# Kernel optimization log

Hardware: AMD Instinct MI355X
Metric: run time of the kernel (lower is better)

## Reference

```python
import jax, jax.numpy as jnp
import numpy as np

B, T, D = 2, 2048, 1024
H, d = 16, 64
INNER = H * d
K = 4  # conv_size
EPS_RMS = 1e-6
EPS_NORM = 1e-12


def _dconv(x, w, b):
    # depthwise causal conv: x (B,T,C), w (C,K), b (C,)
    xp = jnp.pad(x, ((0, 0), (K - 1, 0), (0, 0)))
    Tt = x.shape[1]
    out = b
    for k in range(K):
        out = out + xp[:, k:k + Tt] * w[:, k]
    return out


def _l2norm(x):
    n = jnp.sqrt(jnp.sum(x * x, axis=-1, keepdims=True))
    return x / jnp.maximum(n, EPS_NORM)


def setup_inputs() -> dict:
    key = jax.random.key(0)
    ks = jax.random.split(key, 12)
    s = 0.02
    inp = {
        'x': jax.random.normal(ks[0], (B, T, D), jnp.float32),
        'Wq': jax.random.normal(ks[1], (D, INNER), jnp.float32) * s,
        'Wk': jax.random.normal(ks[2], (D, INNER), jnp.float32) * s,
        'Wv': jax.random.normal(ks[3], (D, INNER), jnp.float32) * s,
        'Wa': jax.random.normal(ks[4], (D, H), jnp.float32) * s,
        'ba': jnp.full((H,), 2.0, jnp.float32),
        'Wb': jax.random.normal(ks[5], (D, H), jnp.float32) * s,
        'bb': jnp.zeros((H,), jnp.float32),
        'Wg': jax.random.normal(ks[6], (D, INNER), jnp.float32) * s,
        'Wo': jax.random.normal(ks[7], (INNER, D), jnp.float32) * s,
        'cq_w': jax.random.normal(ks[8], (INNER, K), jnp.float32) * 0.3,
        'cq_b': jnp.zeros((INNER,), jnp.float32),
        'ck_w': jax.random.normal(ks[9], (INNER, K), jnp.float32) * 0.3,
        'ck_b': jnp.zeros((INNER,), jnp.float32),
        'cv_w': jax.random.normal(ks[10], (INNER, K), jnp.float32) * 0.3,
        'cv_b': jnp.zeros((INNER,), jnp.float32),
        'gamma': jnp.zeros((INNER,), jnp.float32),
    }
    return inp


def reference(x, Wq, Wk, Wv, Wa, ba, Wb, bb, Wg, Wo,
              cq_w, cq_b, ck_w, ck_b, cv_w, cv_b, gamma):
    q = jax.nn.silu(_dconv(x @ Wq, cq_w, cq_b))
    k = jax.nn.silu(_dconv(x @ Wk, ck_w, ck_b))
    v = jax.nn.silu(_dconv(x @ Wv, cv_w, cv_b))
    q = _l2norm(q.reshape(B, T, H, d))
    k = _l2norm(k.reshape(B, T, H, d))
    v = v.reshape(B, T, H, d)
    alpha = jax.nn.sigmoid(x @ Wa + ba)  # (B,T,H)
    beta = jax.nn.sigmoid(x @ Wb + bb)   # (B,T,H)
    gate = jax.nn.silu(x @ Wg)           # (B,T,INNER)

    I_d = jnp.eye(d, dtype=x.dtype)

    def step(S, ins):
        q_t, k_t, v_t, a_t, b_t = ins  # q/k/v: (B,H,d); a,b: (B,H)
        a = a_t[..., None, None]
        b = b_t[..., None, None]
        kkT = k_t[..., :, None] * k_t[..., None, :]   # (B,H,d,d)
        vkT = v_t[..., :, None] * k_t[..., None, :]
        decay = a * (I_d - b * kkT)
        S = jnp.matmul(S, decay) + b * vkT
        o = jnp.einsum('bhde,bhe->bhd', S, q_t)
        return S, o

    # time-major scan inputs
    qT = jnp.transpose(q, (1, 0, 2, 3))
    kT = jnp.transpose(k, (1, 0, 2, 3))
    vT = jnp.transpose(v, (1, 0, 2, 3))
    aT = jnp.transpose(alpha, (1, 0, 2))
    bT = jnp.transpose(beta, (1, 0, 2))
    S0 = jnp.zeros((B, H, d, d), x.dtype)
    _, oT = jax.lax.scan(step, S0, (qT, kT, vT, aT, bT))  # (T,B,H,d)

    out = jnp.transpose(oT, (1, 0, 2, 3)).reshape(B, T, INNER)
    rms = jnp.sqrt(jnp.mean(out * out, axis=-1, keepdims=True) + EPS_RMS)
    out = out / rms * (1.0 + gamma)
    out = out * gate
    return out @ Wo
```

## Files before the change

### kernel.cpp

```cpp
#include <hip/hip_runtime.h>
#include <hip/hip_bf16.h>
#include <cmath>

#define B_ 2
#define T_ 2048
#define D_ 1024
#define H_ 16
#define DH 64
#define INNER_ 1024
#define BT (B_*T_)
#define NCH 32
#define NU (B_*H_*NCH)

typedef __attribute__((ext_vector_type(8))) __bf16 bf16x8;
typedef __attribute__((ext_vector_type(4))) float f32x4;
typedef const __attribute__((address_space(1))) unsigned gas_u32;
typedef __attribute__((address_space(3))) unsigned las_u32;

__device__ __forceinline__ void async16(const void* g, void* l) {
  __builtin_amdgcn_global_load_lds((gas_u32*)g, (las_u32*)l, 16, 0, 0);
}

__device__ __forceinline__ ushort bfr(float x) {
  __hip_bfloat16 t = __float2bfloat16(x);
  return *(ushort*)&t;
}
__device__ __forceinline__ void st_bf4(__hip_bfloat16* p, float a, float b, float c, float d) {
  ushort4 u; u.x = bfr(a); u.y = bfr(b); u.z = bfr(c); u.w = bfr(d);
  *(ushort4*)p = u;
}

__global__ __launch_bounds__(256) void cvt_bf16_kernel(const float* __restrict__ in,
                                                       __hip_bfloat16* __restrict__ out,
                                                       int n4) {
  int i = blockIdx.x * 256 + threadIdx.x;
  if (i >= n4) return;
  float4 v = *(const float4*)(in + (size_t)i * 4);
  __hip_bfloat16 t[4];
  t[0] = __float2bfloat16(v.x); t[1] = __float2bfloat16(v.y);
  t[2] = __float2bfloat16(v.z); t[3] = __float2bfloat16(v.w);
  *(uint2*)(out + (size_t)i * 4) = *(uint2*)t;
}

__global__ __launch_bounds__(256) void transpose_cvt_kernel(const float* __restrict__ in,
                                                            __hip_bfloat16* __restrict__ out,
                                                            int R, int C) {
  __shared__ float tile[32][33];
  const int bc = blockIdx.x * 32, br = blockIdx.y * 32;
  const int tx = threadIdx.x & 31, ty = threadIdx.x >> 5;
#pragma unroll
  for (int i = 0; i < 32; i += 8)
    tile[ty + i][tx] = in[(size_t)(br + ty + i) * C + bc + tx];
  __syncthreads();
#pragma unroll
  for (int i = 0; i < 32; i += 8)
    out[(size_t)(bc + ty + i) * R + br + tx] = __float2bfloat16(tile[tx][ty + i]);
}

__global__ __launch_bounds__(256) void wab_kernel(const float* __restrict__ Wa,
                                                  const float* __restrict__ Wb,
                                                  __hip_bfloat16* __restrict__ Wabt) {
  int idx = blockIdx.x * 256 + threadIdx.x;
  int j = idx >> 10, k = idx & 1023;
  float v = 0.f;
  if (j < 16) v = Wa[k * 16 + j];
  else if (j < 32) v = Wb[k * 16 + (j - 16)];
  Wabt[idx] = __float2bfloat16(v);
}

__global__ __launch_bounds__(256) void gemm_ab(const __hip_bfloat16* __restrict__ A,
                                               const __hip_bfloat16* __restrict__ Bt,
                                               const float* __restrict__ ba,
                                               const float* __restrict__ bb2,
                                               float* __restrict__ alpha,
                                               float* __restrict__ beta, int K) {
  __shared__ __hip_bfloat16 As[128 * 32];
  __shared__ __hip_bfloat16 Bs[128 * 32];
  const int tid = threadIdx.x;
  const int lane = tid & 63, wave = tid >> 6;
  const int wr = wave >> 1, wc = wave & 1;
  const int m0 = blockIdx.y * 128;
  const int srow = tid >> 2, skoff = (tid & 3) * 8;
  const int l15 = lane & 15, lg = lane >> 4;

  f32x4 acc[4][2];
#pragma unroll
  for (int m = 0; m < 4; ++m)
#pragma unroll
    for (int n = 0; n < 2; ++n) acc[m][n] = (f32x4)0.f;

  char* asB = (char*)As;
  char* bsB = (char*)Bs;
  const int ldsw = wave * 1024;

  for (int k0 = 0; k0 < K; k0 += 32) {
    async16(A + (size_t)(m0 + srow) * K + k0 + skoff, asB + ldsw);
    async16(A + (size_t)(m0 + 64 + srow) * K + k0 + skoff, asB + 4096 + ldsw);
    async16(Bt + (size_t)srow * K + k0 + skoff, bsB + ldsw);
    async16(Bt + (size_t)(64 + srow) * K + k0 + skoff, bsB + 4096 + ldsw);
    __syncthreads();
    if (wc == 0) {
      bf16x8 af[4], bfg[2];
#pragma unroll
      for (int m = 0; m < 4; ++m)
        af[m] = *(const bf16x8*)(asB + ((wr * 64 + m * 16 + l15) * 32 + lg * 8) * 2);
#pragma unroll
      for (int n = 0; n < 2; ++n)
        bfg[n] = *(const bf16x8*)(bsB + ((n * 16 + l15) * 32 + lg * 8) * 2);
#pragma unroll
      for (int m = 0; m < 4; ++m)
#pragma unroll
        for (int n = 0; n < 2; ++n)
          acc[m][n] = __builtin_amdgcn_mfma_f32_16x16x32_bf16(af[m], bfg[n], acc[m][n], 0, 0, 0);
    }
    __syncthreads();
  }
  if (wc != 0) return;
#pragma unroll
  for (int m = 0; m < 4; ++m) {
    const int rbase = m0 + wr * 64 + m * 16 + lg * 4;
#pragma unroll
    for (int n = 0; n < 2; ++n) {
      const float bias = (n == 0) ? ba[l15] : bb2[l15];
      float* dst = (n == 0) ? alpha : beta;
#pragma unroll
      for (int r = 0; r < 4; ++r) {
        float vv = acc[m][n][r] + bias;
        dst[(size_t)(rbase + r) * H_ + l15] = 1.f / (1.f + expf(-vv));
      }
    }
  }
}

__device__ __forceinline__ bf16x8 pfrag(const __hip_bfloat16* buf, int row, int ks, int lg) {
  return *(const bf16x8*)((const char*)buf + row * 128 + ks * 64 + lg * 16);
}

__global__ __launch_bounds__(512, 2) void gemm256(const __hip_bfloat16* __restrict__ A,
                                                  const __hip_bfloat16* __restrict__ Bt,
                                                  float* __restrict__ C,
                                                  int M, int N, int K, int act) {
  __shared__ __hip_bfloat16 As[2][256 * 64];
  __shared__ __hip_bfloat16 Bs[2][256 * 64];
  const int tid = threadIdx.x;
  const int lane = tid & 63, wv = tid >> 6;
  const int wr = wv >> 2, wc = wv & 3;
  const int m0 = blockIdx.y * 256, n0 = blockIdx.x * 256;
  const int l15 = lane & 15, lg = lane >> 4;
  const int sr8 = lane >> 3, sc = (lane & 7) * 8;

  f32x4 acc[8][4];
#pragma unroll
  for (int m = 0; m < 8; ++m)
#pragma unroll
    for (int n = 0; n < 4; ++n) acc[m][n] = (f32x4)0.f;

  auto stage = [&](int kt, int bsel) {
    const size_t k0 = (size_t)kt * 64;
    const __hip_bfloat16* Ab = A + (size_t)(m0 + wv * 8 + sr8) * K + k0 + sc;
    const __hip_bfloat16* Bb = Bt + (size_t)(n0 + wv * 8 + sr8) * K + k0 + sc;
    char* al = (char*)As[bsel] + wv * 1024;
    char* bl = (char*)Bs[bsel] + wv * 1024;
#pragma unroll
    for (int q = 0; q < 4; ++q) {
      async16(Ab + (size_t)q * 64 * K, al + q * 8192);
      async16(Bb + (size_t)q * 64 * K, bl + q * 8192);
    }
  };

  const int NT = K >> 6;
  stage(0, 0);
  __syncthreads();
  int cur = 0;
  for (int kt = 0; kt < NT; ++kt) {
    if (kt + 1 < NT) stage(kt + 1, cur ^ 1);
#pragma unroll
    for (int ks = 0; ks < 2; ++ks) {
      bf16x8 af[8], bfg[4];
#pragma unroll
      for (int m = 0; m < 8; ++m)
        af[m] = pfrag(As[cur], wr * 128 + m * 16 + l15, ks, lg);
#pragma unroll
      for (int n = 0; n < 4; ++n)
        bfg[n] = pfrag(Bs[cur], wc * 64 + n * 16 + l15, ks, lg);
#pragma unroll
      for (int m = 0; m < 8; ++m)
#pragma unroll
        for (int n = 0; n < 4; ++n)
          acc[m][n] = __builtin_amdgcn_mfma_f32_16x16x32_bf16(af[m], bfg[n], acc[m][n], 0, 0, 0);
    }
    __syncthreads();
    cur ^= 1;
  }

#pragma unroll
  for (int m = 0; m < 8; ++m) {
    const int rbase = m0 + wr * 128 + m * 16 + lg * 4;
#pragma unroll
    for (int n = 0; n < 4; ++n) {
      const int col = n0 + wc * 64 + n * 16 + l15;
      if (act == 2) {
        const int which = col >> 10;
        const int ncol = col & 1023;
        float* dst = C + (size_t)which * ((size_t)BT * INNER_) +
                     (size_t)rbase * 1024 + ncol;
#pragma unroll
        for (int r = 0; r < 4; ++r) {
          float vv = acc[m][n][r];
          if (which == 3) vv = vv / (1.f + expf(-vv));
          dst[(size_t)r * 1024] = vv;
        }
      } else {
#pragma unroll
        for (int r = 0; r < 4; ++r)
          C[(size_t)(rbase + r) * N + col] = acc[m][n][r];
      }
    }
  }
}

__global__ __launch_bounds__(256) void convnorm_kernel(
    const float* __restrict__ qpre, const float* __restrict__ kpre, const float* __restrict__ vpre,
    const float* __restrict__ cqw, const float* __restrict__ cqb,
    const float* __restrict__ ckw, const float* __restrict__ ckb,
    const float* __restrict__ cvw, const float* __restrict__ cvb,
    float* __restrict__ qn, float* __restrict__ kn, float* __restrict__ vn) {
  const int bt = blockIdx.x;
  const int t = bt & (T_ - 1);
  const int tid = threadIdx.x;
  const int c = tid * 4;

  auto run = [&](const float* __restrict__ pre, const float* __restrict__ w,
                 const float* __restrict__ bias, float* __restrict__ out, bool norm) {
    float r[4];
    float4 bv = *(const float4*)(bias + c);
    r[0] = bv.x; r[1] = bv.y; r[2] = bv.z; r[3] = bv.w;
    float wl[4][4];
#pragma unroll
    for (int i = 0; i < 4; ++i) {
      float4 wv = *(const float4*)(w + (size_t)(c + i) * 4);
      wl[i][0] = wv.x; wl[i][1] = wv.y; wl[i][2] = wv.z; wl[i][3] = wv.w;
    }
#pragma unroll
    for (int kk = 0; kk < 4; ++kk) {
      int tt = t - 3 + kk;
      if (tt >= 0) {
        float4 xv = *(const float4*)(pre + (size_t)(bt - 3 + kk) * INNER_ + c);
        float xa[4] = {xv.x, xv.y, xv.z, xv.w};
#pragma unroll
        for (int i = 0; i < 4; ++i) r[i] += xa[i] * wl[i][kk];
      }
    }
#pragma unroll
    for (int i = 0; i < 4; ++i) r[i] = r[i] / (1.f + expf(-r[i]));
    if (norm) {
      float ss = r[0]*r[0] + r[1]*r[1] + r[2]*r[2] + r[3]*r[3];
      ss += __shfl_xor(ss, 1); ss += __shfl_xor(ss, 2);
      ss += __shfl_xor(ss, 4); ss += __shfl_xor(ss, 8);
      float n = sqrtf(ss);
      float sc = 1.f / fmaxf(n, 1e-12f);
#pragma unroll
      for (int i = 0; i < 4; ++i) r[i] *= sc;
    }
    float4 ov = {r[0], r[1], r[2], r[3]};
    *(float4*)(out + (size_t)bt * INNER_ + c) = ov;
  };

  run(qpre, cqw, cqb, qn, true);
  run(kpre, ckw, ckb, kn, true);
  run(vpre, cvw, cvb, vn, false);
}

#define BST 72

__device__ __forceinline__ bf16x8 fragld(const __hip_bfloat16* buf, int row, int kk, int lg) {
  return *(const bf16x8*)(buf + row * BST + kk * 32 + lg * 8);
}

__global__ __launch_bounds__(256, 2) void precomp_kernel(
    const float* __restrict__ qn, const float* __restrict__ kn, const float* __restrict__ vn,
    const float* __restrict__ alpha, const float* __restrict__ beta,
    __hip_bfloat16* __restrict__ Zg, __hip_bfloat16* __restrict__ G2g,
    float* __restrict__ AVg, float* __restrict__ G1g, float* __restrict__ P63g) {
  __shared__ __hip_bfloat16 sKb[64 * BST], sKip[64 * BST], sKipT[64 * BST];
  __shared__ __hip_bfloat16 sQp[64 * BST], sAttn[64 * BST];
  __shared__ __hip_bfloat16 sXT[128 * BST];
  __shared__ __hip_bfloat16 sM[64 * BST];
  __shared__ float sMd[4][16][16];
  __shared__ float sP[64], sIP[64], sBP[64], sB[64];

  const int u = blockIdx.x;
  const int bh = u >> 5, c = u & 31;
  const int b = bh >> 4, h = bh & 15;
  const int tid = threadIdx.x, lane = tid & 63, wv = tid >> 6;
  const int l15 = lane & 15, lg = lane >> 4;
  const size_t bt0 = (size_t)b * T_ + (size_t)c * 64;
  const size_t hofs = (size_t)h * DH;

  if (wv == 0) {
    float a = alpha[(bt0 + lane) * H_ + h];
    float bb = beta[(bt0 + lane) * H_ + h];
    float la = logf(a);
#pragma unroll
    for (int d = 1; d < 64; d <<= 1) {
      float y = __shfl_up(la, d);
      if (lane >= d) la += y;
    }
    float P = expf(la);
    sP[lane] = P;
    sIP[lane] = 1.f / P;
    sBP[lane] = bb * P;
    sB[lane] = bb;
    if (lane == 63) P63g[u] = P;
  }
  __syncthreads();

#pragma unroll
  for (int i = 0; i < 4; ++i) {
    int e = tid + i * 256;
    int row = e >> 4, c4 = (e & 15) * 4;
    size_t g = (bt0 + row) * INNER_ + hofs + c4;
    float4 kv = *(const float4*)(kn + g);
    float4 qv = *(const float4*)(qn + g);
    float4 vv = *(const float4*)(vn + g);
    float bp = sBP[row], ip = sIP[row], pp = sP[row], bo = sB[row];
    st_bf4(&sKb[row * BST + c4], kv.x * bp, kv.y * bp, kv.z * bp, kv.w * bp);
    st_bf4(&sKip[row * BST + c4], kv.x * ip, kv.y * ip, kv.z * ip, kv.w * ip);
    st_bf4(&sQp[row * BST + c4], qv.x * pp, qv.y * pp, qv.z * pp, qv.w * pp);
    sKipT[(c4 + 0) * BST + row] = __float2bfloat16(kv.x * ip);
    sKipT[(c4 + 1) * BST + row] = __float2bfloat16(kv.y * ip);
    sKipT[(c4 + 2) * BST + row] = __float2bfloat16(kv.z * ip);
    sKipT[(c4 + 3) * BST + row] = __float2bfloat16(kv.w * ip);
    sXT[(c4 + 0) * BST + row] = __float2bfloat16(kv.x * bp);
    sXT[(c4 + 1) * BST + row] = __float2bfloat16(kv.y * bp);
    sXT[(c4 + 2) * BST + row] = __float2bfloat16(kv.z * bp);
    sXT[(c4 + 3) * BST + row] = __float2bfloat16(kv.w * bp);
    sXT[(64 + c4 + 0) * BST + row] = __float2bfloat16(vv.x * bo);
    sXT[(64 + c4 + 1) * BST + row] = __float2bfloat16(vv.y * bo);
    sXT[(64 + c4 + 2) * BST + row] = __float2bfloat16(vv.z * bo);
    sXT[(64 + c4 + 3) * BST + row] = __float2bfloat16(vv.w * bo);
  }
  __syncthreads();

  if (wv < 2) {
#pragma unroll
    for (int tt = wv * 2; tt < wv * 2 + 2; ++tt) {
      for (int n = 0; n <= tt; ++n) {
        f32x4 acc = (f32x4)0.f;
#pragma unroll
        for (int kk = 0; kk < 2; ++kk)
          acc = __builtin_amdgcn_mfma_f32_16x16x32_bf16(
              fragld(sKb, tt * 16 + l15, kk, lg), fragld(sKip, n * 16 + l15, kk, lg), acc, 0, 0, 0);
        if (n < tt) {
#pragma unroll
          for (int q = 0; q < 4; ++q)
            sM[(tt * 16 + lg * 4 + q) * BST + n * 16 + l15] = __float2bfloat16(acc[q]);
        } else {
#pragma unroll
          for (int q = 0; q < 4; ++q) {
            int rr = lg * 4 + q;
            sMd[tt][rr][l15] = (l15 < rr) ? acc[q] : 0.f;
            sM[(tt * 16 + rr) * BST + tt * 16 + l15] = __float2bfloat16(0.f);
          }
        }
      }
    }
  } else {
#pragma unroll
    for (int tt = (wv - 2) * 2; tt < (wv - 2) * 2 + 2; ++tt) {
      for (int n = 0; n < 4; ++n) {
        if (n <= tt) {
          f32x4 acc = (f32x4)0.f;
#pragma unroll
          for (int kk = 0; kk < 2; ++kk)
            acc = __builtin_amdgcn_mfma_f32_16x16x32_bf16(
                fragld(sQp, tt * 16 + l15, kk, lg), fragld(sKip, n * 16 + l15, kk, lg), acc, 0, 0, 0);
#pragma unroll
          for (int q = 0; q < 4; ++q) {
            int r = tt * 16 + lg * 4 + q, cl = n * 16 + l15;
            sAttn[r * BST + cl] = __float2bfloat16((cl <= r) ? acc[q] : 0.f);
          }
        } else {
#pragma unroll
          for (int q = 0; q < 4; ++q)
            sAttn[(tt * 16 + lg * 4 + q) * BST + n * 16 + l15] = __float2bfloat16(0.f);
        }
      }
    }
  }
  __syncthreads();

  auto diag_solve = [&](int I) {
    if (wv < 2) {
      const int cc = wv * 64 + lane;
      float x[16];
#pragma unroll
      for (int t = 0; t < 16; ++t) {
        float r = __bfloat162float(sXT[cc * BST + I * 16 + t]);
#pragma unroll
        for (int s = 0; s < t; ++s) r -= sMd[I][t][s] * x[s];
        x[t] = r;
        sXT[cc * BST + I * 16 + t] = __float2bfloat16(r);
      }
    }
  };

  diag_solve(0);
  __syncthreads();
#pragma unroll
  for (int I = 1; I < 4; ++I) {
    const int KK = (I == 3) ? 2 : 1;
#pragma unroll
    for (int ct2 = 0; ct2 < 2; ++ct2) {
      const int ct = wv * 2 + ct2;
      f32x4 uacc = (f32x4)0.f;
#pragma unroll
      for (int kk = 0; kk < KK; ++kk)
        uacc = __builtin_amdgcn_mfma_f32_16x16x32_bf16(
            fragld(sXT, ct * 16 + l15, kk, lg), fragld(sM, I * 16 + l15, kk, lg), uacc, 0, 0, 0);
#pragma unroll
      for (int q = 0; q < 4; ++q) {
        const int cc = ct * 16 + lg * 4 + q, t = I * 16 + l15;
        float old = __bfloat162float(sXT[cc * BST + t]);
        sXT[cc * BST + t] = __float2bfloat16(old - uacc[q]);
      }
    }
    __syncthreads();
    diag_solve(I);
    __syncthreads();
  }

  const float p63 = sP[63];
  const int tt = wv;
  const size_t go = (size_t)u * 4096;
#pragma unroll
  for (int n = 0; n < 4; ++n) {
    f32x4 av = (f32x4)0.f, aw = (f32x4)0.f, g1 = (f32x4)0.f, g2 = (f32x4)0.f;
#pragma unroll
    for (int kk = 0; kk < 2; ++kk) {
      bf16x8 at = fragld(sAttn, tt * 16 + l15, kk, lg);
      bf16x8 kt = fragld(sKipT, tt * 16 + l15, kk, lg);
      bf16x8 bv = fragld(sXT, 64 + n * 16 + l15, kk, lg);
      bf16x8 bw = fragld(sXT, n * 16 + l15, kk, lg);
      av = __builtin_amdgcn_mfma_f32_16x16x32_bf16(at, bv, av, 0, 0, 0);
      aw = __builtin_amdgcn_mfma_f32_16x16x32_bf16(at, bw, aw, 0, 0, 0);
      g1 = __builtin_amdgcn_mfma_f32_16x16x32_bf16(kt, bv, g1, 0, 0, 0);
      g2 = __builtin_amdgcn_mfma_f32_16x16x32_bf16(kt, bw, g2, 0, 0, 0);
    }
#pragma unroll
    for (int q = 0; q < 4; ++q) {
      int r = tt * 16 + lg * 4 + q, cl = n * 16 + l15;
      AVg[go + r * 64 + cl] = av[q];
      float qp = __bfloat162float(sQp[r * BST + cl]);
      Zg[go + r * 64 + cl] = __float2bfloat16(qp - aw[q]);
      G1g[go + cl * 64 + r] = p63 * g1[q];
      G2g[go + r * 64 + cl] = __float2bfloat16(p63 * g2[q]);
    }
  }
}

__device__ __forceinline__ bf16x8 sfrag(const __hip_bfloat16* buf, int row, int kk, int lg) {
  int byte = row * 128 + kk * 64 + lg * 16;
  byte ^= (row & 7) << 4;
  return *(const bf16x8*)((const char*)buf + byte);
}

__global__ __launch_bounds__(256) void chunkrec_kernel(
    const __hip_bfloat16* __restrict__ Zg, const __hip_bfloat16* __restrict__ G2g,
    const float* __restrict__ AVg, const float* __restrict__ G1g,
    const float* __restrict__ P63g, float* __restrict__ o) {
  __shared__ __align__(16) __hip_bfloat16 sR[16 * 64];
  __shared__ __align__(16) __hip_bfloat16 sZ[2][64 * 64];
  __shared__ __align__(16) __hip_bfloat16 sG2[2][64 * 64];
  const int blk = blockIdx.x;
  const int bh = blk >> 2;
  const int jb = blk & 3;
  const int b = bh >> 4, h = bh & 15;
  const int tid = threadIdx.x, lane = tid & 63, wv = tid >> 6;
  const int l15 = lane & 15, lg = lane >> 4;
  const size_t btb = (size_t)b * T_;
  const size_t hofs = (size_t)h * DH;

  f32x4 R = (f32x4)0.f;

  uint4 zr[2], gr[2];
  const int e0 = tid * 2;

  auto issue = [&](int c) {
    size_t ub = ((size_t)bh * NCH + c) * 4096;
#pragma unroll
    for (int i = 0; i < 2; ++i) {
      zr[i] = *(const uint4*)(Zg + ub + (size_t)(e0 + i) * 8);
      gr[i] = *(const uint4*)(G2g + ub + (size_t)(e0 + i) * 8);
    }
  };
  auto commit = [&](int buf) {
#pragma unroll
    for (int i = 0; i < 2; ++i) {
      int e = e0 + i;
      int row = e >> 3, colb = (e & 7) * 16;
      int byte = (row * 128 + colb) ^ ((row & 7) << 4);
      *(uint4*)((char*)sZ[buf] + byte) = zr[i];
      *(uint4*)((char*)sG2[buf] + byte) = gr[i];
    }
  };

  issue(0);
  commit(0);
  int cur = 0;
  for (int c = 0; c < NCH; ++c) {
#pragma unroll
    for (int q = 0; q < 4; ++q) {
      int i = lg * 4 + q;
      int byte = (i * 128 + (wv * 16 + l15) * 2) ^ ((i & 7) << 4);
      *(__hip_bfloat16*)((char*)sR + byte) = __float2bfloat16(R[q]);
    }
    __syncthreads();

    const size_t ub = ((size_t)bh * NCH + c) * 4096;
    float avr[4], g1r[4];
#pragma unroll
    for (int q = 0; q < 4; ++q) {
      int t = wv * 16 + lg * 4 + q;
      avr[q] = AVg[ub + t * 64 + jb * 16 + l15];
      g1r[q] = G1g[ub + (jb * 16 + lg * 4 + q) * 64 + wv * 16 + l15];
    }
    float p63 = P63g[(size_t)bh * NCH + c];
    if (c + 1 < NCH) issue(c + 1);

    bf16x8 zA[2], rF[2], gB[2];
#pragma unroll
    for (int kk = 0; kk < 2; ++kk) {
      zA[kk] = sfrag(sZ[cur], wv * 16 + l15, kk, lg);
      rF[kk] = sfrag(sR, l15, kk, lg);
      gB[kk] = sfrag(sG2[cur], wv * 16 + l15, kk, lg);
    }
    f32x4 oacc = (f32x4)0.f, gacc = (f32x4)0.f;
#pragma unroll
    for (int kk = 0; kk < 2; ++kk) {
      oacc = __builtin_amdgcn_mfma_f32_16x16x32_bf16(zA[kk], rF[kk], oacc, 0, 0, 0);
      gacc = __builtin_amdgcn_mfma_f32_16x16x32_bf16(rF[kk], gB[kk], gacc, 0, 0, 0);
    }
#pragma unroll
    for (int q = 0; q < 4; ++q) {
      int t = wv * 16 + lg * 4 + q;
      o[(btb + (size_t)c * 64 + t) * INNER_ + hofs + jb * 16 + l15] = avr[q] + oacc[q];
      R[q] = p63 * R[q] + g1r[q] - gacc[q];
    }
    __syncthreads();
    if (c + 1 < NCH) commit(cur ^ 1);
    cur ^= 1;
  }
}

__global__ __launch_bounds__(256) void rmsgate_kernel(const float* __restrict__ o,
    const float* __restrict__ gate, const float* __restrict__ gamma,
    __hip_bfloat16* __restrict__ outn) {
  const int bt = blockIdx.x;
  const int tid = threadIdx.x;
  const size_t base = (size_t)bt * INNER_ + tid * 4;
  float4 ov = *(const float4*)(o + base);
  float ss = ov.x*ov.x + ov.y*ov.y + ov.z*ov.z + ov.w*ov.w;
#pragma unroll
  for (int m = 1; m <= 32; m <<= 1) ss += __shfl_xor(ss, m);
  __shared__ float red[4];
  if ((tid & 63) == 0) red[tid >> 6] = ss;
  __syncthreads();
  float tot = red[0] + red[1] + red[2] + red[3];
  float rms = sqrtf(tot * (1.f / (float)INNER_) + 1e-6f);
  float inv = 1.f / rms;
  float4 gm = *(const float4*)(gamma + tid * 4);
  float4 gt = *(const float4*)(gate + base);
  __hip_bfloat16 t[4];
  t[0] = __float2bfloat16(ov.x * inv * (1.f + gm.x) * gt.x);
  t[1] = __float2bfloat16(ov.y * inv * (1.f + gm.y) * gt.y);
  t[2] = __float2bfloat16(ov.z * inv * (1.f + gm.z) * gt.z);
  t[3] = __float2bfloat16(ov.w * inv * (1.f + gm.w) * gt.w);
  *(uint2*)(outn + base) = *(uint2*)t;
}

extern "C" void kernel_launch(void* const* d_in, const int* in_sizes, int n_in,
                              void* d_out, int out_size, void* d_ws, size_t ws_size,
                              hipStream_t stream) {
  const float* x   = (const float*)d_in[0];
  const float* Wq  = (const float*)d_in[1];
  const float* Wk  = (const float*)d_in[2];
  const float* Wv  = (const float*)d_in[3];
  const float* Wa  = (const float*)d_in[4];
  const float* ba  = (const float*)d_in[5];
  const float* Wb  = (const float*)d_in[6];
  const float* bb  = (const float*)d_in[7];
  const float* Wg  = (const float*)d_in[8];
  const float* Wo  = (const float*)d_in[9];
  const float* cqw = (const float*)d_in[10];
  const float* cqb = (const float*)d_in[11];
  const float* ckw = (const float*)d_in[12];
  const float* ckb = (const float*)d_in[13];
  const float* cvw = (const float*)d_in[14];
  const float* cvb = (const float*)d_in[15];
  const float* gamma = (const float*)d_in[16];

  float* ws = (float*)d_ws;
  const size_t N1 = (size_t)BT * INNER_;
  float* qpre = ws;
  float* kpre = ws + N1;
  float* vpre = ws + 2 * N1;
  float* gate = ws + 3 * N1;
  float* qn   = ws + 4 * N1;
  float* kn   = ws + 5 * N1;
  float* vn   = ws + 6 * N1;
  float* alpha = ws + 7 * N1;
  float* beta  = alpha + (size_t)BT * H_;
  __hip_bfloat16* wt0 = (__hip_bfloat16*)(beta + (size_t)BT * H_);
  __hip_bfloat16* Wot = wt0 + 4 * (size_t)D_ * INNER_;
  float* P63s = (float*)(Wot + (size_t)D_ * INNER_);
  __hip_bfloat16* Wabt = (__hip_bfloat16*)(P63s + NU);
  __hip_bfloat16* xb  = (__hip_bfloat16*)vn;
  float* AVg = qpre;
  __hip_bfloat16* Zg  = (__hip_bfloat16*)kpre;
  __hip_bfloat16* G2g = Zg + (size_t)NU * 4096;
  float* G1g = vpre;
  float* obuf = qn;
  __hip_bfloat16* nrmb = (__hip_bfloat16*)kn;
  float* outp = (float*)d_out;

  cvt_bf16_kernel<<<(BT * D_ / 4 + 255) / 256, 256, 0, stream>>>(x, xb, BT * D_ / 4);
  dim3 tgrid(INNER_ / 32, D_ / 32);
  transpose_cvt_kernel<<<tgrid, 256, 0, stream>>>(Wq, wt0, D_, INNER_);
  transpose_cvt_kernel<<<tgrid, 256, 0, stream>>>(Wk, wt0 + (size_t)D_ * INNER_, D_, INNER_);
  transpose_cvt_kernel<<<tgrid, 256, 0, stream>>>(Wv, wt0 + 2 * (size_t)D_ * INNER_, D_, INNER_);
  transpose_cvt_kernel<<<tgrid, 256, 0, stream>>>(Wg, wt0 + 3 * (size_t)D_ * INNER_, D_, INNER_);
  transpose_cvt_kernel<<<dim3(D_ / 32, INNER_ / 32), 256, 0, stream>>>(Wo, Wot, INNER_, D_);
  wab_kernel<<<(128 * 1024) / 256, 256, 0, stream>>>(Wa, Wb, Wabt);

  gemm256<<<dim3(4 * INNER_ / 256, BT / 256), 512, 0, stream>>>(
      xb, wt0, qpre, BT, 4 * INNER_, D_, 2);
  gemm_ab<<<dim3(1, BT / 128), 256, 0, stream>>>(xb, Wabt, ba, bb, alpha, beta, D_);

  convnorm_kernel<<<BT, 256, 0, stream>>>(qpre, kpre, vpre, cqw, cqb, ckw, ckb,
                                          cvw, cvb, qn, kn, vn);

  precomp_kernel<<<NU, 256, 0, stream>>>(qn, kn, vn, alpha, beta, Zg, G2g, AVg, G1g, P63s);
  chunkrec_kernel<<<B_ * H_ * 4, 256, 0, stream>>>(Zg, G2g, AVg, G1g, P63s, obuf);

  rmsgate_kernel<<<BT, 256, 0, stream>>>(obuf, gate, gamma, nrmb);

  gemm256<<<dim3(D_ / 256, BT / 256), 512, 0, stream>>>(nrmb, Wot, outp, BT, D_, INNER_, 0);
}
```

Before: 371.0 us.

## Fuse prep kernels, alpha/beta GEMM, and conv-norm into neighbors; store bf16 intermediates

Merges the input/weight conversion kernels into one prep launch. The alpha/beta projection becomes an extra column tile of the main QKVG GEMM, and the depthwise conv + SiLU + L2 norm moves into precomp_kernel. Q/K/V/gate pre-activations are now stored as bf16 instead of fp32, which cuts intermediate memory traffic and launch count. In exchange, the conv reads extra halo rows, the GEMM spends a mostly wasted 256-column tile on 32 useful columns, and bf16 rounding before the conv lowers precision.

```diff
diff --git a/kernel.cpp b/kernel.cpp
--- a/kernel.cpp
+++ b/kernel.cpp
@@ -11,6 +11,7 @@
 #define BT (B_*T_)
 #define NCH 32
 #define NU (B_*H_*NCH)
+#define N1 ((size_t)BT * INNER_)
 
 typedef __attribute__((ext_vector_type(8))) __bf16 bf16x8;
 typedef __attribute__((ext_vector_type(4))) float f32x4;
@@ -29,107 +30,48 @@
   ushort4 u; u.x = bfr(a); u.y = bfr(b); u.z = bfr(c); u.w = bfr(d);
   *(ushort4*)p = u;
 }
-
-__global__ __launch_bounds__(256) void cvt_bf16_kernel(const float* __restrict__ in,
-                                                       __hip_bfloat16* __restrict__ out,
-                                                       int n4) {
-  int i = blockIdx.x * 256 + threadIdx.x;
-  if (i >= n4) return;
-  float4 v = *(const float4*)(in + (size_t)i * 4);
-  __hip_bfloat16 t[4];
-  t[0] = __float2bfloat16(v.x); t[1] = __float2bfloat16(v.y);
-  t[2] = __float2bfloat16(v.z); t[3] = __float2bfloat16(v.w);
-  *(uint2*)(out + (size_t)i * 4) = *(uint2*)t;
-}
-
-__global__ __launch_bounds__(256) void transpose_cvt_kernel(const float* __restrict__ in,
-                                                            __hip_bfloat16* __restrict__ out,
-                                                            int R, int C) {
+__device__ __forceinline__ float b2f(ushort s) {
+  return __uint_as_float(((unsigned)s) << 16);
+}
+
+__global__ __launch_bounds__(256) void prep_kernel(
+    const float* __restrict__ x,
+    const float* __restrict__ Wq, const float* __restrict__ Wk,
+    const float* __restrict__ Wv, const float* __restrict__ Wg,
+    const float* __restrict__ Wo, const float* __restrict__ Wa,
+    const float* __restrict__ Wb,
+    __hip_bfloat16* __restrict__ xb, __hip_bfloat16* __restrict__ wtall,
+    __hip_bfloat16* __restrict__ Wot) {
   __shared__ float tile[32][33];
-  const int bc = blockIdx.x * 32, br = blockIdx.y * 32;
-  const int tx = threadIdx.x & 31, ty = threadIdx.x >> 5;
-#pragma unroll
-  for (int i = 0; i < 32; i += 8)
-    tile[ty + i][tx] = in[(size_t)(br + ty + i) * C + bc + tx];
-  __syncthreads();
-#pragma unroll
-  for (int i = 0; i < 32; i += 8)
-    out[(size_t)(bc + ty + i) * R + br + tx] = __float2bfloat16(tile[tx][ty + i]);
-}
-
-__global__ __launch_bounds__(256) void wab_kernel(const float* __restrict__ Wa,
-                                                  const float* __restrict__ Wb,
-                                                  __hip_bfloat16* __restrict__ Wabt) {
-  int idx = blockIdx.x * 256 + threadIdx.x;
-  int j = idx >> 10, k = idx & 1023;
+  const int bid = blockIdx.x, tid = threadIdx.x;
+  if (bid < 4096) {
+    int i = bid * 256 + tid;
+    float4 v = *(const float4*)(x + (size_t)i * 4);
+    st_bf4(xb + (size_t)i * 4, v.x, v.y, v.z, v.w);
+    return;
+  }
+  if (bid < 9216) {
+    int wi = (bid - 4096) >> 10;
+    int t = (bid - 4096) & 1023;
+    const float* src = wi == 0 ? Wq : wi == 1 ? Wk : wi == 2 ? Wv : wi == 3 ? Wg : Wo;
+    __hip_bfloat16* dst = (wi < 4) ? (wtall + (size_t)wi * 1024 * 1024) : Wot;
+    const int bc = (t & 31) * 32, br = (t >> 5) * 32;
+    const int tx = tid & 31, ty = tid >> 5;
+#pragma unroll
+    for (int i2 = 0; i2 < 32; i2 += 8)
+      tile[ty + i2][tx] = src[(size_t)(br + ty + i2) * 1024 + bc + tx];
+    __syncthreads();
+#pragma unroll
+    for (int i2 = 0; i2 < 32; i2 += 8)
+      dst[(size_t)(bc + ty + i2) * 1024 + br + tx] = __float2bfloat16(tile[tx][ty + i2]);
+    return;
+  }
+  int idx = (bid - 9216) * 256 + tid;
+  int j = idx >> 10, k2 = idx & 1023;
   float v = 0.f;
-  if (j < 16) v = Wa[k * 16 + j];
-  else if (j < 32) v = Wb[k * 16 + (j - 16)];
-  Wabt[idx] = __float2bfloat16(v);
-}
-
-__global__ __launch_bounds__(256) void gemm_ab(const __hip_bfloat16* __restrict__ A,
-                                               const __hip_bfloat16* __restrict__ Bt,
-                                               const float* __restrict__ ba,
-                                               const float* __restrict__ bb2,
-                                               float* __restrict__ alpha,
-                                               float* __restrict__ beta, int K) {
-  __shared__ __hip_bfloat16 As[128 * 32];
-  __shared__ __hip_bfloat16 Bs[128 * 32];
-  const int tid = threadIdx.x;
-  const int lane = tid & 63, wave = tid >> 6;
-  const int wr = wave >> 1, wc = wave & 1;
-  const int m0 = blockIdx.y * 128;
-  const int srow = tid >> 2, skoff = (tid & 3) * 8;
-  const int l15 = lane & 15, lg = lane >> 4;
-
-  f32x4 acc[4][2];
-#pragma unroll
-  for (int m = 0; m < 4; ++m)
-#pragma unroll
-    for (int n = 0; n < 2; ++n) acc[m][n] = (f32x4)0.f;
-
-  char* asB = (char*)As;
-  char* bsB = (char*)Bs;
-  const int ldsw = wave * 1024;
-
-  for (int k0 = 0; k0 < K; k0 += 32) {
-    async16(A + (size_t)(m0 + srow) * K + k0 + skoff, asB + ldsw);
-    async16(A + (size_t)(m0 + 64 + srow) * K + k0 + skoff, asB + 4096 + ldsw);
-    async16(Bt + (size_t)srow * K + k0 + skoff, bsB + ldsw);
-    async16(Bt + (size_t)(64 + srow) * K + k0 + skoff, bsB + 4096 + ldsw);
-    __syncthreads();
-    if (wc == 0) {
-      bf16x8 af[4], bfg[2];
-#pragma unroll
-      for (int m = 0; m < 4; ++m)
-        af[m] = *(const bf16x8*)(asB + ((wr * 64 + m * 16 + l15) * 32 + lg * 8) * 2);
-#pragma unroll
-      for (int n = 0; n < 2; ++n)
-        bfg[n] = *(const bf16x8*)(bsB + ((n * 16 + l15) * 32 + lg * 8) * 2);
-#pragma unroll
-      for (int m = 0; m < 4; ++m)
-#pragma unroll
-        for (int n = 0; n < 2; ++n)
-          acc[m][n] = __builtin_amdgcn_mfma_f32_16x16x32_bf16(af[m], bfg[n], acc[m][n], 0, 0, 0);
-    }
-    __syncthreads();
-  }
-  if (wc != 0) return;
-#pragma unroll
-  for (int m = 0; m < 4; ++m) {
-    const int rbase = m0 + wr * 64 + m * 16 + lg * 4;
-#pragma unroll
-    for (int n = 0; n < 2; ++n) {
-      const float bias = (n == 0) ? ba[l15] : bb2[l15];
-      float* dst = (n == 0) ? alpha : beta;
-#pragma unroll
-      for (int r = 0; r < 4; ++r) {
-        float vv = acc[m][n][r] + bias;
-        dst[(size_t)(rbase + r) * H_ + l15] = 1.f / (1.f + expf(-vv));
-      }
-    }
-  }
+  if (j < 16) v = Wa[k2 * 16 + j];
+  else if (j < 32) v = Wb[k2 * 16 + (j - 16)];
+  wtall[(size_t)4096 * 1024 + idx] = __float2bfloat16(v);
 }
 
 __device__ __forceinline__ bf16x8 pfrag(const __hip_bfloat16* buf, int row, int ks, int lg) {
@@ -138,7 +80,12 @@
 
 __global__ __launch_bounds__(512, 2) void gemm256(const __hip_bfloat16* __restrict__ A,
                                                   const __hip_bfloat16* __restrict__ Bt,
-                                                  float* __restrict__ C,
+                                                  float* __restrict__ Cf,
+                                                  __hip_bfloat16* __restrict__ Cb,
+                                                  float* __restrict__ alpha,
+                                                  float* __restrict__ beta,
+                                                  const float* __restrict__ ba,
+                                                  const float* __restrict__ bb2,
                                                   int M, int N, int K, int act) {
   __shared__ __hip_bfloat16 As[2][256 * 64];
   __shared__ __hip_bfloat16 Bs[2][256 * 64];
@@ -200,86 +147,48 @@
     for (int n = 0; n < 4; ++n) {
       const int col = n0 + wc * 64 + n * 16 + l15;
       if (act == 2) {
-        const int which = col >> 10;
-        const int ncol = col & 1023;
-        float* dst = C + (size_t)which * ((size_t)BT * INNER_) +
-                     (size_t)rbase * 1024 + ncol;
-#pragma unroll
-        for (int r = 0; r < 4; ++r) {
-          float vv = acc[m][n][r];
-          if (which == 3) vv = vv / (1.f + expf(-vv));
-          dst[(size_t)r * 1024] = vv;
+        if (col < 4096) {
+          const int which = col >> 10;
+          const int ncol = col & 1023;
+          __hip_bfloat16* dst = Cb + (size_t)which * N1 + (size_t)rbase * 1024 + ncol;
+#pragma unroll
+          for (int r = 0; r < 4; ++r) {
+            float vv = acc[m][n][r];
+            if (which == 3) vv = vv / (1.f + expf(-vv));
+            dst[(size_t)r * 1024] = __float2bfloat16(vv);
+          }
+        } else {
+          const int ncol = col - 4096;
+          if (ncol < 32) {
+            const float bias = (ncol < 16) ? ba[ncol] : bb2[ncol - 16];
+            float* dst = (ncol < 16) ? (alpha + ncol) : (beta + (ncol - 16));
+#pragma unroll
+            for (int r = 0; r < 4; ++r)
+              dst[(size_t)(rbase + r) * H_] = 1.f / (1.f + expf(-(acc[m][n][r] + bias)));
+          }
         }
       } else {
 #pragma unroll
         for (int r = 0; r < 4; ++r)
-          C[(size_t)(rbase + r) * N + col] = acc[m][n][r];
+          Cf[(size_t)(rbase + r) * N + col] = acc[m][n][r];
       }
     }
   }
 }
 
-__global__ __launch_bounds__(256) void convnorm_kernel(
-    const float* __restrict__ qpre, const float* __restrict__ kpre, const float* __restrict__ vpre,
+#define BST 72
+
+__device__ __forceinline__ bf16x8 fragld(const __hip_bfloat16* buf, int row, int kk, int lg) {
+  return *(const bf16x8*)(buf + row * BST + kk * 32 + lg * 8);
+}
+
+__global__ __launch_bounds__(256, 2) void precomp_kernel(
+    const __hip_bfloat16* __restrict__ qpre, const __hip_bfloat16* __restrict__ kpre,
+    const __hip_bfloat16* __restrict__ vpre,
+    const float* __restrict__ alpha, const float* __restrict__ beta,
     const float* __restrict__ cqw, const float* __restrict__ cqb,
     const float* __restrict__ ckw, const float* __restrict__ ckb,
     const float* __restrict__ cvw, const float* __restrict__ cvb,
-    float* __restrict__ qn, float* __restrict__ kn, float* __restrict__ vn) {
-  const int bt = blockIdx.x;
-  const int t = bt & (T_ - 1);
-  const int tid = threadIdx.x;
-  const int c = tid * 4;
-
-  auto run = [&](const float* __restrict__ pre, const float* __restrict__ w,
-                 const float* __restrict__ bias, float* __restrict__ out, bool norm) {
-    float r[4];
-    float4 bv = *(const float4*)(bias + c);
-    r[0] = bv.x; r[1] = bv.y; r[2] = bv.z; r[3] = bv.w;
-    float wl[4][4];
-#pragma unroll
-    for (int i = 0; i < 4; ++i) {
-      float4 wv = *(const float4*)(w + (size_t)(c + i) * 4);
-      wl[i][0] = wv.x; wl[i][1] = wv.y; wl[i][2] = wv.z; wl[i][3] = wv.w;
-    }
-#pragma unroll
-    for (int kk = 0; kk < 4; ++kk) {
-      int tt = t - 3 + kk;
-      if (tt >= 0) {
-        float4 xv = *(const float4*)(pre + (size_t)(bt - 3 + kk) * INNER_ + c);
-        float xa[4] = {xv.x, xv.y, xv.z, xv.w};
-#pragma unroll
-        for (int i = 0; i < 4; ++i) r[i] += xa[i] * wl[i][kk];
-      }
-    }
-#pragma unroll
-    for (int i = 0; i < 4; ++i) r[i] = r[i] / (1.f + expf(-r[i]));
-    if (norm) {
-      float ss = r[0]*r[0] + r[1]*r[1] + r[2]*r[2] + r[3]*r[3];
-      ss += __shfl_xor(ss, 1); ss += __shfl_xor(ss, 2);
-      ss += __shfl_xor(ss, 4); ss += __shfl_xor(ss, 8);
-      float n = sqrtf(ss);
-      float sc = 1.f / fmaxf(n, 1e-12f);
-#pragma unroll
-      for (int i = 0; i < 4; ++i) r[i] *= sc;
-    }
-    float4 ov = {r[0], r[1], r[2], r[3]};
-    *(float4*)(out + (size_t)bt * INNER_ + c) = ov;
-  };
-
-  run(qpre, cqw, cqb, qn, true);
-  run(kpre, ckw, ckb, kn, true);
-  run(vpre, cvw, cvb, vn, false);
-}
-
-#define BST 72
-
-__device__ __forceinline__ bf16x8 fragld(const __hip_bfloat16* buf, int row, int kk, int lg) {
-  return *(const bf16x8*)(buf + row * BST + kk * 32 + lg * 8);
-}
-
-__global__ __launch_bounds__(256, 2) void precomp_kernel(
-    const float* __restrict__ qn, const float* __restrict__ kn, const float* __restrict__ vn,
-    const float* __restrict__ alpha, const float* __restrict__ beta,
     __hip_bfloat16* __restrict__ Zg, __hip_bfloat16* __restrict__ G2g,
     float* __restrict__ AVg, float* __restrict__ G1g, float* __restrict__ P63g) {
   __shared__ __hip_bfloat16 sKb[64 * BST], sKip[64 * BST], sKipT[64 * BST];
@@ -319,26 +228,69 @@
   for (int i = 0; i < 4; ++i) {
     int e = tid + i * 256;
     int row = e >> 4, c4 = (e & 15) * 4;
-    size_t g = (bt0 + row) * INNER_ + hofs + c4;
-    float4 kv = *(const float4*)(kn + g);
-    float4 qv = *(const float4*)(qn + g);
-    float4 vv = *(const float4*)(vn + g);
+    int gc = (int)hofs + c4;
+    int tseq = c * 64 + row;
+    float rq[4], rk[4], rv[4];
+    {
+      float4 bq = *(const float4*)(cqb + gc);
+      float4 bk = *(const float4*)(ckb + gc);
+      float4 bv = *(const float4*)(cvb + gc);
+      rq[0] = bq.x; rq[1] = bq.y; rq[2] = bq.z; rq[3] = bq.w;
+      rk[0] = bk.x; rk[1] = bk.y; rk[2] = bk.z; rk[3] = bk.w;
+      rv[0] = bv.x; rv[1] = bv.y; rv[2] = bv.z; rv[3] = bv.w;
+    }
+    float wq[4][4], wk[4][4], wvv[4][4];
+#pragma unroll
+    for (int j = 0; j < 4; ++j) {
+      float4 a4 = *(const float4*)(cqw + (size_t)(gc + j) * 4);
+      wq[j][0] = a4.x; wq[j][1] = a4.y; wq[j][2] = a4.z; wq[j][3] = a4.w;
+      float4 b4 = *(const float4*)(ckw + (size_t)(gc + j) * 4);
+      wk[j][0] = b4.x; wk[j][1] = b4.y; wk[j][2] = b4.z; wk[j][3] = b4.w;
+      float4 c4v = *(const float4*)(cvw + (size_t)(gc + j) * 4);
+      wvv[j][0] = c4v.x; wvv[j][1] = c4v.y; wvv[j][2] = c4v.z; wvv[j][3] = c4v.w;
+    }
+#pragma unroll
+    for (int kk = 0; kk < 4; ++kk) {
+      if (tseq - 3 + kk >= 0) {
+        size_t off = (bt0 + row - 3 + kk) * INNER_ + gc;
+        ushort4 uq = *(const ushort4*)(qpre + off);
+        ushort4 uk = *(const ushort4*)(kpre + off);
+        ushort4 uv = *(const ushort4*)(vpre + off);
+        rq[0] += b2f(uq.x) * wq[0][kk]; rq[1] += b2f(uq.y) * wq[1][kk];
+        rq[2] += b2f(uq.z) * wq[2][kk]; rq[3] += b2f(uq.w) * wq[3][kk];
+        rk[0] += b2f(uk.x) * wk[0][kk]; rk[1] += b2f(uk.y) * wk[1][kk];
+        rk[2] += b2f(uk.z) * wk[2][kk]; rk[3] += b2f(uk.w) * wk[3][kk];
+        rv[0] += b2f(uv.x) * wvv[0][kk]; rv[1] += b2f(uv.y) * wvv[1][kk];
+        rv[2] += b2f(uv.z) * wvv[2][kk]; rv[3] += b2f(uv.w) * wvv[3][kk];
+      }
+    }
+#pragma unroll
+    for (int j = 0; j < 4; ++j) {
+      rq[j] = rq[j] / (1.f + expf(-rq[j]));
+      rk[j] = rk[j] / (1.f + expf(-rk[j]));
+      rv[j] = rv[j] / (1.f + expf(-rv[j]));
+    }
+    float ssq = rq[0]*rq[0] + rq[1]*rq[1] + rq[2]*rq[2] + rq[3]*rq[3];
+    float ssk = rk[0]*rk[0] + rk[1]*rk[1] + rk[2]*rk[2] + rk[3]*rk[3];
+    ssq += __shfl_xor(ssq, 1); ssq += __shfl_xor(ssq, 2);
+    ssq += __shfl_xor(ssq, 4); ssq += __shfl_xor(ssq, 8);
+    ssk += __shfl_xor(ssk, 1); ssk += __shfl_xor(ssk, 2);
+    ssk += __shfl_xor(ssk, 4); ssk += __shfl_xor(ssk, 8);
+    float scq = 1.f / fmaxf(sqrtf(ssq), 1e-12f);
+    float sck = 1.f / fmaxf(sqrtf(ssk), 1e-12f);
+#pragma unroll
+    for (int j = 0; j < 4; ++j) { rq[j] *= scq; rk[j] *= sck; }
+
     float bp = sBP[row], ip = sIP[row], pp = sP[row], bo = sB[row];
-    st_bf4(&sKb[row * BST + c4], kv.x * bp, kv.y * bp, kv.z * bp, kv.w * bp);
-    st_bf4(&sKip[row * BST + c4], kv.x * ip, kv.y * ip, kv.z * ip, kv.w * ip);
-    st_bf4(&sQp[row * BST + c4], qv.x * pp, qv.y * pp, qv.z * pp, qv.w * pp);
-    sKipT[(c4 + 0) * BST + row] = __float2bfloat16(kv.x * ip);
-    sKipT[(c4 + 1) * BST + row] = __float2bfloat16(kv.y * ip);
-    sKipT[(c4 + 2) * BST + row] = __float2bfloat16(kv.z * ip);
-    sKipT[(c4 + 3) * BST + row] = __float2bfloat16(kv.w * ip);
-    sXT[(c4 + 0) * BST + row] = __float2bfloat16(kv.x * bp);
-    sXT[(c4 + 1) * BST + row] = __float2bfloat16(kv.y * bp);
-    sXT[(c4 + 2) * BST + row] = __float2bfloat16(kv.z * bp);
-    sXT[(c4 + 3) * BST + row] = __float2bfloat16(kv.w * bp);
-    sXT[(64 + c4 + 0) * BST + row] = __float2bfloat16(vv.x * bo);
-    sXT[(64 + c4 + 1) * BST + row] = __float2bfloat16(vv.y * bo);
-    sXT[(64 + c4 + 2) * BST + row] = __float2bfloat16(vv.z * bo);
-    sXT[(64 + c4 + 3) * BST + row] = __float2bfloat16(vv.w * bo);
+    st_bf4(&sKb[row * BST + c4], rk[0] * bp, rk[1] * bp, rk[2] * bp, rk[3] * bp);
+    st_bf4(&sKip[row * BST + c4], rk[0] * ip, rk[1] * ip, rk[2] * ip, rk[3] * ip);
+    st_bf4(&sQp[row * BST + c4], rq[0] * pp, rq[1] * pp, rq[2] * pp, rq[3] * pp);
+#pragma unroll
+    for (int j = 0; j < 4; ++j) {
+      sKipT[(c4 + j) * BST + row] = __float2bfloat16(rk[j] * ip);
+      sXT[(c4 + j) * BST + row] = __float2bfloat16(rk[j] * bp);
+      sXT[(64 + c4 + j) * BST + row] = __float2bfloat16(rv[j] * bo);
+    }
   }
   __syncthreads();
 
@@ -554,7 +506,7 @@
 }
 
 __global__ __launch_bounds__(256) void rmsgate_kernel(const float* __restrict__ o,
-    const float* __restrict__ gate, const float* __restrict__ gamma,
+    const __hip_bfloat16* __restrict__ gate, const float* __restrict__ gamma,
     __hip_bfloat16* __restrict__ outn) {
   const int bt = blockIdx.x;
   const int tid = threadIdx.x;
@@ -570,13 +522,12 @@
   float rms = sqrtf(tot * (1.f / (float)INNER_) + 1e-6f);
   float inv = 1.f / rms;
   float4 gm = *(const float4*)(gamma + tid * 4);
-  float4 gt = *(const float4*)(gate + base);
-  __hip_bfloat16 t[4];
-  t[0] = __float2bfloat16(ov.x * inv * (1.f + gm.x) * gt.x);
-  t[1] = __float2bfloat16(ov.y * inv * (1.f + gm.y) * gt.y);
-  t[2] = __float2bfloat16(ov.z * inv * (1.f + gm.z) * gt.z);
-  t[3] = __float2bfloat16(ov.w * inv * (1.f + gm.w) * gt.w);
-  *(uint2*)(outn + base) = *(uint2*)t;
+  ushort4 gt = *(const ushort4*)(gate + base);
+  st_bf4(outn + base,
+         ov.x * inv * (1.f + gm.x) * b2f(gt.x),
+         ov.y * inv * (1.f + gm.y) * b2f(gt.y),
+         ov.z * inv * (1.f + gm.z) * b2f(gt.z),
+         ov.w * inv * (1.f + gm.w) * b2f(gt.w));
 }
 
 extern "C" void kernel_launch(void* const* d_in, const int* in_sizes, int n_in,
@@ -600,50 +551,33 @@
   const float* cvb = (const float*)d_in[15];
   const float* gamma = (const float*)d_in[16];
 
-  float* ws = (float*)d_ws;
-  const size_t N1 = (size_t)BT * INNER_;
-  float* qpre = ws;
-  float* kpre = ws + N1;
-  float* vpre = ws + 2 * N1;
-  float* gate = ws + 3 * N1;
-  float* qn   = ws + 4 * N1;
-  float* kn   = ws + 5 * N1;
-  float* vn   = ws + 6 * N1;
-  float* alpha = ws + 7 * N1;
-  float* beta  = alpha + (size_t)BT * H_;
-  __hip_bfloat16* wt0 = (__hip_bfloat16*)(beta + (size_t)BT * H_);
-  __hip_bfloat16* Wot = wt0 + 4 * (size_t)D_ * INNER_;
-  float* P63s = (float*)(Wot + (size_t)D_ * INNER_);
-  __hip_bfloat16* Wabt = (__hip_bfloat16*)(P63s + NU);
-  __hip_bfloat16* xb  = (__hip_bfloat16*)vn;
-  float* AVg = qpre;
-  __hip_bfloat16* Zg  = (__hip_bfloat16*)kpre;
-  __hip_bfloat16* G2g = Zg + (size_t)NU * 4096;
-  float* G1g = vpre;
-  float* obuf = qn;
-  __hip_bfloat16* nrmb = (__hip_bfloat16*)kn;
+  char* p = (char*)d_ws;
+  __hip_bfloat16* qkvg = (__hip_bfloat16*)p;  p += 4 * N1 * 2;
+  __hip_bfloat16* xb   = (__hip_bfloat16*)p;  p += N1 * 2;
+  float* alpha = (float*)p;  p += (size_t)BT * H_ * 4;
+  float* beta  = (float*)p;  p += (size_t)BT * H_ * 4;
+  __hip_bfloat16* wtall = (__hip_bfloat16*)p;  p += (size_t)4352 * 1024 * 2;
+  __hip_bfloat16* Wot   = (__hip_bfloat16*)p;  p += (size_t)1024 * 1024 * 2;
+  float* AVg = (float*)p;  p += (size_t)NU * 4096 * 4;
+  float* G1g = (float*)p;  p += (size_t)NU * 4096 * 4;
+  __hip_bfloat16* Zg  = (__hip_bfloat16*)p;  p += (size_t)NU * 4096 * 2;
+  __hip_bfloat16* G2g = (__hip_bfloat16*)p;  p += (size_t)NU * 4096 * 2;
+  float* obuf = (float*)p;  p += N1 * 4;
+  float* P63s = (float*)p;  p += (size_t)NU * 4;
+  __hip_bfloat16* nrmb = xb;
   float* outp = (float*)d_out;
 
-  cvt_bf16_kernel<<<(BT * D_ / 4 + 255) / 256, 256, 0, stream>>>(x, xb, BT * D_ / 4);
-  dim3 tgrid(INNER_ / 32, D_ / 32);
-  transpose_cvt_kernel<<<tgrid, 256, 0, stream>>>(Wq, wt0, D_, INNER_);
-  transpose_cvt_kernel<<<tgrid, 256, 0, stream>>>(Wk, wt0 + (size_t)D_ * INNER_, D_, INNER_);
-  transpose_cvt_kernel<<<tgrid, 256, 0, stream>>>(Wv, wt0 + 2 * (size_t)D_ * INNER_, D_, INNER_);
-  transpose_cvt_kernel<<<tgrid, 256, 0, stream>>>(Wg, wt0 + 3 * (size_t)D_ * INNER_, D_, INNER_);
-  transpose_cvt_kernel<<<dim3(D_ / 32, INNER_ / 32), 256, 0, stream>>>(Wo, Wot, INNER_, D_);
-  wab_kernel<<<(128 * 1024) / 256, 256, 0, stream>>>(Wa, Wb, Wabt);
-
-  gemm256<<<dim3(4 * INNER_ / 256, BT / 256), 512, 0, stream>>>(
-      xb, wt0, qpre, BT, 4 * INNER_, D_, 2);
-  gemm_ab<<<dim3(1, BT / 128), 256, 0, stream>>>(xb, Wabt, ba, bb, alpha, beta, D_);
-
-  convnorm_kernel<<<BT, 256, 0, stream>>>(qpre, kpre, vpre, cqw, cqb, ckw, ckb,
-                                          cvw, cvb, qn, kn, vn);
-
-  precomp_kernel<<<NU, 256, 0, stream>>>(qn, kn, vn, alpha, beta, Zg, G2g, AVg, G1g, P63s);
+  prep_kernel<<<10240, 256, 0, stream>>>(x, Wq, Wk, Wv, Wg, Wo, Wa, Wb, xb, wtall, Wot);
+
+  gemm256<<<dim3(17, BT / 256), 512, 0, stream>>>(
+      xb, wtall, nullptr, qkvg, alpha, beta, ba, bb, BT, 4352, D_, 2);
+
+  precomp_kernel<<<NU, 256, 0, stream>>>(qkvg, qkvg + N1, qkvg + 2 * N1,
+                                         alpha, beta, cqw, cqb, ckw, ckb, cvw, cvb,
+                                         Zg, G2g, AVg, G1g, P63s);
   chunkrec_kernel<<<B_ * H_ * 4, 256, 0, stream>>>(Zg, G2g, AVg, G1g, P63s, obuf);
 
-  rmsgate_kernel<<<BT, 256, 0, stream>>>(obuf, gate, gamma, nrmb);
-
-  gemm256<<<dim3(D_ / 256, BT / 256), 512, 0, stream>>>(nrmb, Wot, outp, BT, D_, INNER_, 0);
-}
+  rmsgate_kernel<<<BT, 256, 0, stream>>>(obuf, qkvg + 3 * N1, gamma, nrmb);
+  gemm256<<<dim3(D_ / 256, BT / 256), 512, 0, stream>>>(
+      nrmb, Wot, outp, nullptr, nullptr, nullptr, nullptr, nullptr, BT, D_, INNER_, 0);
+}
```

Measured after the change: 365.1 us. No clear change (-1.6%).
